# Kernel tuning notes

Measured on AMD Instinct MI355X. Metric: run time of the kernel, lower is better.

## Reference

```python
import jax, jax.numpy as jnp
import numpy as np

BN_EPS = 1e-5


def _guide_net(fullres, w1, b1, bn_gamma, bn_beta, bn_mean, bn_var, w2, b2):
    # two 1x1 convs == channel matmuls
    x = jnp.einsum('nchw,oc->nohw', fullres, w1[:, :, 0, 0]) + b1[None, :, None, None]
    inv = bn_gamma / jnp.sqrt(bn_var + BN_EPS)
    x = (x - bn_mean[None, :, None, None]) * inv[None, :, None, None] + bn_beta[None, :, None, None]
    x = jax.nn.relu(x)
    g = jnp.einsum('nchw,oc->nohw', x, w2[:, :, 0, 0]) + b2[None, :, None, None]
    return jax.nn.sigmoid(g)  # [N,1,H,W] in (0,1)


def _slice_one(grid_n, guide_n):
    # grid_n: [C,D,h,w]; guide_n: [H,W]; trilinear grid_sample, align_corners=True.
    C, D, h, w = grid_n.shape
    H, W = guide_n.shape
    # normalized coords in torch code map exactly to voxel coords [0, size-1]
    gz = guide_n * (D - 1)                      # per-pixel depth coord [H,W]
    z0f = jnp.floor(gz)
    tz = (gz - z0f)[None, :, :]                 # [1,H,W]
    z0 = jnp.clip(z0f, 0, D - 1).astype(jnp.int32)
    z1 = jnp.clip(z0f + 1, 0, D - 1).astype(jnp.int32)
    gy = jnp.linspace(0.0, h - 1.0, H)
    y0f = jnp.floor(gy)
    ty = (gy - y0f)[None, :, None]              # [1,H,1]
    y0 = jnp.clip(y0f, 0, h - 1).astype(jnp.int32)[:, None]
    y1 = jnp.clip(y0f + 1, 0, h - 1).astype(jnp.int32)[:, None]
    gx = jnp.linspace(0.0, w - 1.0, W)
    x0f = jnp.floor(gx)
    tx = (gx - x0f)[None, None, :]              # [1,1,W]
    x0 = jnp.clip(x0f, 0, w - 1).astype(jnp.int32)[None, :]
    x1 = jnp.clip(x0f + 1, 0, w - 1).astype(jnp.int32)[None, :]

    def g(z, y, x):
        # z:[H,W], y:[H,1], x:[1,W] -> broadcast gather -> [C,H,W]
        return grid_n[:, z, y, x]

    def lerp_xy(z):
        a = g(z, y0, x0) * (1 - tx) + g(z, y0, x1) * tx
        b = g(z, y1, x0) * (1 - tx) + g(z, y1, x1) * tx
        return a * (1 - ty) + b * ty

    return lerp_xy(z0) * (1 - tz) + lerp_xy(z1) * tz  # [C,H,W]


def _apply_coeffs(coeff, fullres):
    # coeff: [N,12,H,W]; rows (0:3,+3), (4:7,+7), (8:11,+11)
    N, _, H, W = coeff.shape
    A = coeff[:, jnp.array([0, 1, 2, 4, 5, 6, 8, 9, 10])].reshape(N, 3, 3, H, W)
    bias = coeff[:, jnp.array([3, 7, 11])]
    return jnp.einsum('nkchw,nchw->nkhw', A, fullres) + bias


def setup_inputs() -> dict:
    key = jax.random.key(0)
    ks = jax.random.split(key, 10)
    N, H, W = 2, 1080, 1920
    return {
        'fullres': jax.random.uniform(ks[0], (N, 3, H, W), jnp.float32),
        'bilateral_grid': jax.random.normal(ks[1], (N, 12, 8, 16, 16), jnp.float32),
        'w1': jax.random.normal(ks[2], (16, 3, 1, 1), jnp.float32) * 0.2,
        'b1': jax.random.normal(ks[3], (16,), jnp.float32) * 0.1,
        'bn_gamma': jax.random.uniform(ks[4], (16,), jnp.float32, 0.5, 1.5),
        'bn_beta': jax.random.normal(ks[5], (16,), jnp.float32) * 0.1,
        'bn_mean': jax.random.normal(ks[6], (16,), jnp.float32) * 0.1,
        'bn_var': jax.random.uniform(ks[7], (16,), jnp.float32, 0.5, 1.5),
        'w2': jax.random.normal(ks[8], (1, 16, 1, 1), jnp.float32) * 0.2,
        'b2': jax.random.normal(ks[9], (1,), jnp.float32) * 0.1,
    }


def reference(fullres, bilateral_grid, w1, b1, bn_gamma, bn_beta, bn_mean, bn_var, w2, b2):
    guide = _guide_net(fullres, w1, b1, bn_gamma, bn_beta, bn_mean, bn_var, w2, b2)  # [N,1,H,W]
    coeff = jax.vmap(_slice_one)(bilateral_grid, guide[:, 0])                         # [N,12,H,W]
    return _apply_coeffs(coeff, fullres)                                              # [N,3,H,W]
```

## Files before the change

### kernel.cpp

```cpp
#include <hip/hip_runtime.h>
#include <hip/hip_bf16.h>
#include <math.h>

#define HWV (1080 * 1920)

typedef _Float16 half2 __attribute__((ext_vector_type(2)));
typedef __fp16   pk2   __attribute__((ext_vector_type(2)));
union U32H2 { unsigned u; half2 h; pk2 p; };

__global__ void prep_w(const float* __restrict__ w1, const float* __restrict__ b1,
                       const float* __restrict__ gamma, const float* __restrict__ beta,
                       const float* __restrict__ mean, const float* __restrict__ var,
                       const float* __restrict__ w2, const float* __restrict__ b2,
                       float* __restrict__ wsw) {
    int i = threadIdx.x;
    if (i < 16) {
        float inv = gamma[i] / sqrtf(var[i] + 1e-5f);
        float wr = w1[i*3+0] * inv, wg = w1[i*3+1] * inv, wb = w1[i*3+2] * inv;
        float bs = (b1[i] - mean[i]) * inv + beta[i];
        wsw[64 + i] = w2[i];
        unsigned* wp = (unsigned*)(wsw + 84);
        U32H2 t;
        t.p = __builtin_amdgcn_cvt_pkrtz(wr, wr); wp[i*4+0] = t.u;
        t.p = __builtin_amdgcn_cvt_pkrtz(wg, wg); wp[i*4+1] = t.u;
        t.p = __builtin_amdgcn_cvt_pkrtz(wb, wb); wp[i*4+2] = t.u;
        t.p = __builtin_amdgcn_cvt_pkrtz(bs, bs); wp[i*4+3] = t.u;
    }
    if (i == 0) wsw[80] = b2[0];
}

__global__ __launch_bounds__(512, 8) void fused_kernel(
        const float* __restrict__ fullres,
        const float* __restrict__ grid,
        const float* __restrict__ wsw,
        float* __restrict__ out) {
    __shared__ unsigned slo[9][9][4];
    __shared__ unsigned shi[9][9][2];

    const int tid = threadIdx.x;
    const int n   = blockIdx.z;
    const int y   = blockIdx.y;
    const int xs  = blockIdx.x * 1024;
    const int x   = xs + 2 * tid;
    const bool act = (x < 1920);

    const int p = y * 1920 + min(x, 1918);
    const float* fr = fullres + n * 3 * HWV + p;
    float2 R = *(const float2*)(fr);
    float2 G = *(const float2*)(fr + HWV);
    float2 B = *(const float2*)(fr + 2 * HWV);

    const int a = (int)((float)xs * (15.0f / 1919.0f));
    {
        float gy = (float)y * (15.0f / 1079.0f);
        float y0f = floorf(gy);
        float ty = gy - y0f;
        int y0 = min((int)y0f, 15);
        int y1 = min(y0 + 1, 15);
        const int dy = (y1 - y0) * 16;
        const float* gb = grid + n * 24576 + y0 * 16;
        if (tid < 486) {
            int j   = tid / 81;
            int rem = tid - j * 81;
            int z   = rem / 9;
            int k   = rem - z * 9;
            int zz  = min(z, 7);
            int xc  = min(a + k, 15);
            const float* q0 = gb + (2 * j) * 2048 + zz * 256 + xc;
            const float* q1 = q0 + 2048;
            float v00 = q0[0], v01 = q0[dy];
            float v10 = q1[0], v11 = q1[dy];
            float e0 = fmaf(ty, v01 - v00, v00);
            float e1 = fmaf(ty, v11 - v10, v10);
            U32H2 t;
            t.p = __builtin_amdgcn_cvt_pkrtz(e0, e1);
            if (j < 4) slo[k][z][j] = t.u;
            else       shi[k][z][j - 4] = t.u;
        }
    }
    __syncthreads();

    if (!act) return;

    U32H2 rr, gg, bb;
    rr.p = __builtin_amdgcn_cvt_pkrtz(R.x, R.y);
    gg.p = __builtin_amdgcn_cvt_pkrtz(G.x, G.y);
    bb.p = __builtin_amdgcn_cvt_pkrtz(B.x, B.y);
    const unsigned* wp = (const unsigned*)(wsw + 84);
    const half2 zero = {(_Float16)0.0f, (_Float16)0.0f};
    float b2s = wsw[80];
    float acc0 = b2s, acc1 = b2s;
#pragma unroll
    for (int c = 0; c < 16; ++c) {
        U32H2 wr, wg, wb, bs;
        wr.u = wp[4*c+0]; wg.u = wp[4*c+1]; wb.u = wp[4*c+2]; bs.u = wp[4*c+3];
        half2 h = wr.h * rr.h + (wg.h * gg.h + (wb.h * bb.h + bs.h));
        h = __builtin_elementwise_max(h, zero);
        float w2c = wsw[64 + c];
        acc0 = fmaf((float)h.x, w2c, acc0);
        acc1 = fmaf((float)h.y, w2c, acc1);
    }

    float accv[2] = {acc0, acc1};
    float rv[2] = {R.x, R.y}, gv[2] = {G.x, G.y}, bv[2] = {B.x, B.y};
    float outr[2], outg[2], outb[2];

#pragma unroll
    for (int q = 0; q < 2; ++q) {
        float e = __expf(-accv[q]);
        float guide = __builtin_amdgcn_rcpf(1.0f + e);
        float gz = guide * 7.0f;
        float z0f = floorf(gz);
        float tz = gz - z0f;
        int z0 = min((int)z0f, 7);
        int z1 = z0 + 1;

        float gx = (float)(x + q) * (15.0f / 1919.0f);
        float x0f = floorf(gx);
        float tx = gx - x0f;
        int x0 = (int)x0f;
        int k0 = x0 - a;
        int k1 = min(x0 + 1, 15) - a;

        float wx0 = 1.0f - tx, wx1 = tx;
        float wz0 = 1.0f - tz, wz1 = tz;

        U32H2 w00h, w01h, w10h, w11h;
        w00h.p = __builtin_amdgcn_cvt_pkrtz(wx0 * wz0, wx0 * wz0);
        w01h.p = __builtin_amdgcn_cvt_pkrtz(wx0 * wz1, wx0 * wz1);
        w10h.p = __builtin_amdgcn_cvt_pkrtz(wx1 * wz0, wx1 * wz0);
        w11h.p = __builtin_amdgcn_cvt_pkrtz(wx1 * wz1, wx1 * wz1);

        const uint4 A0 = *(const uint4*)&slo[k0][z0][0];
        const uint4 A1 = *(const uint4*)&slo[k0][z1][0];
        const uint4 B0 = *(const uint4*)&slo[k1][z0][0];
        const uint4 B1 = *(const uint4*)&slo[k1][z1][0];
        const uint2 C0 = *(const uint2*)&shi[k0][z0][0];
        const uint2 C1 = *(const uint2*)&shi[k0][z1][0];
        const uint2 D0 = *(const uint2*)&shi[k1][z0][0];
        const uint2 D1 = *(const uint2*)&shi[k1][z1][0];

        unsigned a0j[6] = {A0.x, A0.y, A0.z, A0.w, C0.x, C0.y};
        unsigned a1j[6] = {A1.x, A1.y, A1.z, A1.w, C1.x, C1.y};
        unsigned b0j[6] = {B0.x, B0.y, B0.z, B0.w, D0.x, D0.y};
        unsigned b1j[6] = {B1.x, B1.y, B1.z, B1.w, D1.x, D1.y};

        half2 hc[6];
#pragma unroll
        for (int j = 0; j < 6; ++j) {
            U32H2 ua0, ua1, ub0, ub1;
            ua0.u = a0j[j]; ua1.u = a1j[j]; ub0.u = b0j[j]; ub1.u = b1j[j];
            half2 h = w00h.h * ua0.h + (w01h.h * ua1.h);
            h = w10h.h * ub0.h + h;
            h = w11h.h * ub1.h + h;
            hc[j] = h;
        }

        outr[q] = fmaf((float)hc[0].x, rv[q], fmaf((float)hc[0].y, gv[q],
                  fmaf((float)hc[1].x, bv[q], (float)hc[1].y)));
        outg[q] = fmaf((float)hc[2].x, rv[q], fmaf((float)hc[2].y, gv[q],
                  fmaf((float)hc[3].x, bv[q], (float)hc[3].y)));
        outb[q] = fmaf((float)hc[4].x, rv[q], fmaf((float)hc[4].y, gv[q],
                  fmaf((float)hc[5].x, bv[q], (float)hc[5].y)));
    }

    float* op = out + n * 3 * HWV + p;
    *(float2*)(op)           = make_float2(outr[0], outr[1]);
    *(float2*)(op + HWV)     = make_float2(outg[0], outg[1]);
    *(float2*)(op + 2 * HWV) = make_float2(outb[0], outb[1]);
}

extern "C" void kernel_launch(void* const* d_in, const int* in_sizes, int n_in,
                              void* d_out, int out_size, void* d_ws, size_t ws_size,
                              hipStream_t stream) {
    const float* fullres = (const float*)d_in[0];
    const float* grid    = (const float*)d_in[1];
    const float* w1      = (const float*)d_in[2];
    const float* b1      = (const float*)d_in[3];
    const float* gamma   = (const float*)d_in[4];
    const float* beta    = (const float*)d_in[5];
    const float* mean    = (const float*)d_in[6];
    const float* var     = (const float*)d_in[7];
    const float* w2      = (const float*)d_in[8];
    const float* b2      = (const float*)d_in[9];
    float* out = (float*)d_out;

    float* wsw = (float*)d_ws;

    prep_w<<<1, 64, 0, stream>>>(w1, b1, gamma, beta, mean, var, w2, b2, wsw);

    dim3 grid_dim(2, 1080, 2);
    fused_kernel<<<grid_dim, 512, 0, stream>>>(fullres, grid, wsw, out);
}
```

Baseline: 32.25 us.

## Process four rows per block with double-buffered grid slice and prefetch

Each block now handles four image rows instead of one. While computing the current row, it prefetches the next row's pixels and grid samples into a second shared-memory buffer. This amortizes block launch and setup, and hides global load latency behind compute. In exchange there are four times fewer blocks, an extra barrier per row, and more register pressure from the prefetched values.

```diff
diff --git a/kernel.cpp b/kernel.cpp
--- a/kernel.cpp
+++ b/kernel.cpp
@@ -3,6 +3,7 @@
 #include <math.h>
 
 #define HWV (1080 * 1920)
+#define NROWS 4
 
 typedef _Float16 half2 __attribute__((ext_vector_type(2)));
 typedef __fp16   pk2   __attribute__((ext_vector_type(2)));
@@ -34,140 +35,178 @@
         const float* __restrict__ grid,
         const float* __restrict__ wsw,
         float* __restrict__ out) {
-    __shared__ unsigned slo[9][9][4];
-    __shared__ unsigned shi[9][9][2];
+    __shared__ unsigned slo[2][9][9][4];
+    __shared__ unsigned shi[2][9][9][2];
 
     const int tid = threadIdx.x;
-    const int n   = blockIdx.z;
-    const int y   = blockIdx.y;
-    const int xs  = blockIdx.x * 1024;
+    const int seg = blockIdx.x;
+    const int n   = blockIdx.y;
+    const int yb  = blockIdx.z * NROWS;
+    const int xs  = seg * 1024;
     const int x   = xs + 2 * tid;
     const bool act = (x < 1920);
-
-    const int p = y * 1920 + min(x, 1918);
-    const float* fr = fullres + n * 3 * HWV + p;
-    float2 R = *(const float2*)(fr);
-    float2 G = *(const float2*)(fr + HWV);
-    float2 B = *(const float2*)(fr + 2 * HWV);
-
     const int a = (int)((float)xs * (15.0f / 1919.0f));
-    {
+    const int pcol = min(x, 1918);
+
+    const bool sact = (tid < 486);
+    int sj = 0, sz = 0, sk = 0;
+    const float* sq0 = grid;
+    if (sact) {
+        sj = tid / 81;
+        int rem = tid - sj * 81;
+        sz = rem / 9;
+        sk = rem - sz * 9;
+        int szz = min(sz, 7);
+        int sxc = min(a + sk, 15);
+        sq0 = grid + n * 24576 + (2 * sj) * 2048 + szz * 256 + sxc;
+    }
+
+    float sv0, sv1, sv2, sv3, sty;
+    auto stage_load = [&](int y) {
         float gy = (float)y * (15.0f / 1079.0f);
         float y0f = floorf(gy);
-        float ty = gy - y0f;
+        sty = gy - y0f;
         int y0 = min((int)y0f, 15);
         int y1 = min(y0 + 1, 15);
-        const int dy = (y1 - y0) * 16;
-        const float* gb = grid + n * 24576 + y0 * 16;
-        if (tid < 486) {
-            int j   = tid / 81;
-            int rem = tid - j * 81;
-            int z   = rem / 9;
-            int k   = rem - z * 9;
-            int zz  = min(z, 7);
-            int xc  = min(a + k, 15);
-            const float* q0 = gb + (2 * j) * 2048 + zz * 256 + xc;
-            const float* q1 = q0 + 2048;
-            float v00 = q0[0], v01 = q0[dy];
-            float v10 = q1[0], v11 = q1[dy];
-            float e0 = fmaf(ty, v01 - v00, v00);
-            float e1 = fmaf(ty, v11 - v10, v10);
+        if (sact) {
+            const float* q0 = sq0 + y0 * 16;
+            int dy = (y1 - y0) * 16;
+            sv0 = q0[0];    sv1 = q0[dy];
+            sv2 = q0[2048]; sv3 = q0[2048 + dy];
+        }
+    };
+    auto stage_write = [&](int buf) {
+        if (sact) {
+            float e0 = fmaf(sty, sv1 - sv0, sv0);
+            float e1 = fmaf(sty, sv3 - sv2, sv2);
             U32H2 t;
             t.p = __builtin_amdgcn_cvt_pkrtz(e0, e1);
-            if (j < 4) slo[k][z][j] = t.u;
-            else       shi[k][z][j - 4] = t.u;
-        }
-    }
-    __syncthreads();
-
-    if (!act) return;
-
-    U32H2 rr, gg, bb;
-    rr.p = __builtin_amdgcn_cvt_pkrtz(R.x, R.y);
-    gg.p = __builtin_amdgcn_cvt_pkrtz(G.x, G.y);
-    bb.p = __builtin_amdgcn_cvt_pkrtz(B.x, B.y);
+            if (sj < 4) slo[buf][sk][sz][sj] = t.u;
+            else        shi[buf][sk][sz][sj - 4] = t.u;
+        }
+    };
+    auto fr_load = [&](int y, float2& R, float2& G, float2& B) {
+        const float* fr = fullres + n * 3 * HWV + y * 1920 + pcol;
+        R = *(const float2*)(fr);
+        G = *(const float2*)(fr + HWV);
+        B = *(const float2*)(fr + 2 * HWV);
+    };
+
     const unsigned* wp = (const unsigned*)(wsw + 84);
     const half2 zero = {(_Float16)0.0f, (_Float16)0.0f};
-    float b2s = wsw[80];
-    float acc0 = b2s, acc1 = b2s;
-#pragma unroll
-    for (int c = 0; c < 16; ++c) {
-        U32H2 wr, wg, wb, bs;
-        wr.u = wp[4*c+0]; wg.u = wp[4*c+1]; wb.u = wp[4*c+2]; bs.u = wp[4*c+3];
-        half2 h = wr.h * rr.h + (wg.h * gg.h + (wb.h * bb.h + bs.h));
-        h = __builtin_elementwise_max(h, zero);
-        float w2c = wsw[64 + c];
-        acc0 = fmaf((float)h.x, w2c, acc0);
-        acc1 = fmaf((float)h.y, w2c, acc1);
+    const float b2s = wsw[80];
+
+    float2 R, G, B;
+    stage_load(yb);
+    fr_load(yb, R, G, B);
+    stage_write(0);
+    __syncthreads();
+
+    int cur = 0;
+#pragma unroll
+    for (int rrow = 0; rrow < NROWS; ++rrow) {
+        const int y = yb + rrow;
+        const int p = y * 1920 + pcol;
+
+        float2 Rn, Gn, Bn;
+        if (rrow + 1 < NROWS) {
+            stage_load(y + 1);
+            fr_load(y + 1, Rn, Gn, Bn);
+        }
+
+        if (act) {
+            U32H2 rr, gg, bb;
+            rr.p = __builtin_amdgcn_cvt_pkrtz(R.x, R.y);
+            gg.p = __builtin_amdgcn_cvt_pkrtz(G.x, G.y);
+            bb.p = __builtin_amdgcn_cvt_pkrtz(B.x, B.y);
+            float acc0 = b2s, acc1 = b2s;
+#pragma unroll
+            for (int c = 0; c < 16; ++c) {
+                U32H2 wr, wg, wb, bs;
+                wr.u = wp[4*c+0]; wg.u = wp[4*c+1]; wb.u = wp[4*c+2]; bs.u = wp[4*c+3];
+                half2 h = wr.h * rr.h + (wg.h * gg.h + (wb.h * bb.h + bs.h));
+                h = __builtin_elementwise_max(h, zero);
+                float w2c = wsw[64 + c];
+                acc0 = fmaf((float)h.x, w2c, acc0);
+                acc1 = fmaf((float)h.y, w2c, acc1);
+            }
+
+            float accv[2] = {acc0, acc1};
+            float rv[2] = {R.x, R.y}, gv[2] = {G.x, G.y}, bv[2] = {B.x, B.y};
+            float outr[2], outg[2], outb[2];
+
+#pragma unroll
+            for (int q = 0; q < 2; ++q) {
+                float e = __expf(-accv[q]);
+                float guide = __builtin_amdgcn_rcpf(1.0f + e);
+                float gz = guide * 7.0f;
+                float z0f = floorf(gz);
+                float tz = gz - z0f;
+                int z0 = min((int)z0f, 7);
+                int z1 = z0 + 1;
+
+                float gx = (float)(x + q) * (15.0f / 1919.0f);
+                float x0f = floorf(gx);
+                float tx = gx - x0f;
+                int x0 = (int)x0f;
+                int k0 = x0 - a;
+                int k1 = min(x0 + 1, 15) - a;
+
+                float wx0 = 1.0f - tx, wx1 = tx;
+                float wz0 = 1.0f - tz, wz1 = tz;
+
+                U32H2 w00h, w01h, w10h, w11h;
+                w00h.p = __builtin_amdgcn_cvt_pkrtz(wx0 * wz0, wx0 * wz0);
+                w01h.p = __builtin_amdgcn_cvt_pkrtz(wx0 * wz1, wx0 * wz1);
+                w10h.p = __builtin_amdgcn_cvt_pkrtz(wx1 * wz0, wx1 * wz0);
+                w11h.p = __builtin_amdgcn_cvt_pkrtz(wx1 * wz1, wx1 * wz1);
+
+                const uint4 A0 = *(const uint4*)&slo[cur][k0][z0][0];
+                const uint4 A1 = *(const uint4*)&slo[cur][k0][z1][0];
+                const uint4 B0 = *(const uint4*)&slo[cur][k1][z0][0];
+                const uint4 B1 = *(const uint4*)&slo[cur][k1][z1][0];
+                const uint2 C0 = *(const uint2*)&shi[cur][k0][z0][0];
+                const uint2 C1 = *(const uint2*)&shi[cur][k0][z1][0];
+                const uint2 D0 = *(const uint2*)&shi[cur][k1][z0][0];
+                const uint2 D1 = *(const uint2*)&shi[cur][k1][z1][0];
+
+                unsigned a0j[6] = {A0.x, A0.y, A0.z, A0.w, C0.x, C0.y};
+                unsigned a1j[6] = {A1.x, A1.y, A1.z, A1.w, C1.x, C1.y};
+                unsigned b0j[6] = {B0.x, B0.y, B0.z, B0.w, D0.x, D0.y};
+                unsigned b1j[6] = {B1.x, B1.y, B1.z, B1.w, D1.x, D1.y};
+
+                half2 hc[6];
+#pragma unroll
+                for (int j = 0; j < 6; ++j) {
+                    U32H2 ua0, ua1, ub0, ub1;
+                    ua0.u = a0j[j]; ua1.u = a1j[j]; ub0.u = b0j[j]; ub1.u = b1j[j];
+                    half2 h = w00h.h * ua0.h + (w01h.h * ua1.h);
+                    h = w10h.h * ub0.h + h;
+                    h = w11h.h * ub1.h + h;
+                    hc[j] = h;
+                }
+
+                outr[q] = fmaf((float)hc[0].x, rv[q], fmaf((float)hc[0].y, gv[q],
+                          fmaf((float)hc[1].x, bv[q], (float)hc[1].y)));
+                outg[q] = fmaf((float)hc[2].x, rv[q], fmaf((float)hc[2].y, gv[q],
+                          fmaf((float)hc[3].x, bv[q], (float)hc[3].y)));
+                outb[q] = fmaf((float)hc[4].x, rv[q], fmaf((float)hc[4].y, gv[q],
+                          fmaf((float)hc[5].x, bv[q], (float)hc[5].y)));
+            }
+
+            float* op = out + n * 3 * HWV + p;
+            *(float2*)(op)           = make_float2(outr[0], outr[1]);
+            *(float2*)(op + HWV)     = make_float2(outg[0], outg[1]);
+            *(float2*)(op + 2 * HWV) = make_float2(outb[0], outb[1]);
+        }
+
+        if (rrow + 1 < NROWS) {
+            stage_write(cur ^ 1);
+        }
+        __syncthreads();
+        cur ^= 1;
+        R = Rn; G = Gn; B = Bn;
     }
-
-    float accv[2] = {acc0, acc1};
-    float rv[2] = {R.x, R.y}, gv[2] = {G.x, G.y}, bv[2] = {B.x, B.y};
-    float outr[2], outg[2], outb[2];
-
-#pragma unroll
-    for (int q = 0; q < 2; ++q) {
-        float e = __expf(-accv[q]);
-        float guide = __builtin_amdgcn_rcpf(1.0f + e);
-        float gz = guide * 7.0f;
-        float z0f = floorf(gz);
-        float tz = gz - z0f;
-        int z0 = min((int)z0f, 7);
-        int z1 = z0 + 1;
-
-        float gx = (float)(x + q) * (15.0f / 1919.0f);
-        float x0f = floorf(gx);
-        float tx = gx - x0f;
-        int x0 = (int)x0f;
-        int k0 = x0 - a;
-        int k1 = min(x0 + 1, 15) - a;
-
-        float wx0 = 1.0f - tx, wx1 = tx;
-        float wz0 = 1.0f - tz, wz1 = tz;
-
-        U32H2 w00h, w01h, w10h, w11h;
-        w00h.p = __builtin_amdgcn_cvt_pkrtz(wx0 * wz0, wx0 * wz0);
-        w01h.p = __builtin_amdgcn_cvt_pkrtz(wx0 * wz1, wx0 * wz1);
-        w10h.p = __builtin_amdgcn_cvt_pkrtz(wx1 * wz0, wx1 * wz0);
-        w11h.p = __builtin_amdgcn_cvt_pkrtz(wx1 * wz1, wx1 * wz1);
-
-        const uint4 A0 = *(const uint4*)&slo[k0][z0][0];
-        const uint4 A1 = *(const uint4*)&slo[k0][z1][0];
-        const uint4 B0 = *(const uint4*)&slo[k1][z0][0];
-        const uint4 B1 = *(const uint4*)&slo[k1][z1][0];
-        const uint2 C0 = *(const uint2*)&shi[k0][z0][0];
-        const uint2 C1 = *(const uint2*)&shi[k0][z1][0];
-        const uint2 D0 = *(const uint2*)&shi[k1][z0][0];
-        const uint2 D1 = *(const uint2*)&shi[k1][z1][0];
-
-        unsigned a0j[6] = {A0.x, A0.y, A0.z, A0.w, C0.x, C0.y};
-        unsigned a1j[6] = {A1.x, A1.y, A1.z, A1.w, C1.x, C1.y};
-        unsigned b0j[6] = {B0.x, B0.y, B0.z, B0.w, D0.x, D0.y};
-        unsigned b1j[6] = {B1.x, B1.y, B1.z, B1.w, D1.x, D1.y};
-
-        half2 hc[6];
-#pragma unroll
-        for (int j = 0; j < 6; ++j) {
-            U32H2 ua0, ua1, ub0, ub1;
-            ua0.u = a0j[j]; ua1.u = a1j[j]; ub0.u = b0j[j]; ub1.u = b1j[j];
-            half2 h = w00h.h * ua0.h + (w01h.h * ua1.h);
-            h = w10h.h * ub0.h + h;
-            h = w11h.h * ub1.h + h;
-            hc[j] = h;
-        }
-
-        outr[q] = fmaf((float)hc[0].x, rv[q], fmaf((float)hc[0].y, gv[q],
-                  fmaf((float)hc[1].x, bv[q], (float)hc[1].y)));
-        outg[q] = fmaf((float)hc[2].x, rv[q], fmaf((float)hc[2].y, gv[q],
-                  fmaf((float)hc[3].x, bv[q], (float)hc[3].y)));
-        outb[q] = fmaf((float)hc[4].x, rv[q], fmaf((float)hc[4].y, gv[q],
-                  fmaf((float)hc[5].x, bv[q], (float)hc[5].y)));
-    }
-
-    float* op = out + n * 3 * HWV + p;
-    *(float2*)(op)           = make_float2(outr[0], outr[1]);
-    *(float2*)(op + HWV)     = make_float2(outg[0], outg[1]);
-    *(float2*)(op + 2 * HWV) = make_float2(outb[0], outb[1]);
 }
 
 extern "C" void kernel_launch(void* const* d_in, const int* in_sizes, int n_in,
@@ -189,6 +228,6 @@
 
     prep_w<<<1, 64, 0, stream>>>(w1, b1, gamma, beta, mean, var, w2, b2, wsw);
 
-    dim3 grid_dim(2, 1080, 2);
+    dim3 grid_dim(2, 2, 1080 / NROWS);
     fused_kernel<<<grid_dim, 512, 0, stream>>>(fullres, grid, wsw, out);
 }
```

Result: slower. 35.86 us (+11.2%).

## Process one full image row per 960-thread block instead of two half-row blocks

Applied to the files above, without the earlier changes.

Each block now covers a whole 1920-pixel row with 960 threads, so the grid goes from 2x1080x2 blocks of 512 threads to 1080x2 blocks. The shared y-interpolated grid slice grows to all 16 x columns, filled by 864 threads, and the per-block x offset and the inactive-thread early exit are removed. This halves the per-block grid staging and removes the wasted threads in the second half-row block. In exchange, blocks are larger, the occupancy hint is dropped, and each block does more staging work before its barrier.

```diff
diff --git a/kernel.cpp b/kernel.cpp
--- a/kernel.cpp
+++ b/kernel.cpp
@@ -29,28 +29,25 @@
     if (i == 0) wsw[80] = b2[0];
 }
 
-__global__ __launch_bounds__(512, 8) void fused_kernel(
+__global__ __launch_bounds__(960) void fused_kernel(
         const float* __restrict__ fullres,
         const float* __restrict__ grid,
         const float* __restrict__ wsw,
         float* __restrict__ out) {
-    __shared__ unsigned slo[9][9][4];
-    __shared__ unsigned shi[9][9][2];
+    __shared__ unsigned slo[16][9][4];
+    __shared__ unsigned shi[16][9][2];
 
     const int tid = threadIdx.x;
-    const int n   = blockIdx.z;
-    const int y   = blockIdx.y;
-    const int xs  = blockIdx.x * 1024;
-    const int x   = xs + 2 * tid;
-    const bool act = (x < 1920);
+    const int y   = blockIdx.x;
+    const int n   = blockIdx.y;
+    const int x   = 2 * tid;
+    const int p   = y * 1920 + x;
 
-    const int p = y * 1920 + min(x, 1918);
     const float* fr = fullres + n * 3 * HWV + p;
     float2 R = *(const float2*)(fr);
     float2 G = *(const float2*)(fr + HWV);
     float2 B = *(const float2*)(fr + 2 * HWV);
 
-    const int a = (int)((float)xs * (15.0f / 1919.0f));
     {
         float gy = (float)y * (15.0f / 1079.0f);
         float y0f = floorf(gy);
@@ -59,14 +56,13 @@
         int y1 = min(y0 + 1, 15);
         const int dy = (y1 - y0) * 16;
         const float* gb = grid + n * 24576 + y0 * 16;
-        if (tid < 486) {
-            int j   = tid / 81;
-            int rem = tid - j * 81;
-            int z   = rem / 9;
-            int k   = rem - z * 9;
+        if (tid < 864) {
+            int k   = tid / 54;
+            int rem = tid - k * 54;
+            int z   = rem / 6;
+            int j   = rem - z * 6;
             int zz  = min(z, 7);
-            int xc  = min(a + k, 15);
-            const float* q0 = gb + (2 * j) * 2048 + zz * 256 + xc;
+            const float* q0 = gb + (2 * j) * 2048 + zz * 256 + k;
             const float* q1 = q0 + 2048;
             float v00 = q0[0], v01 = q0[dy];
             float v10 = q1[0], v11 = q1[dy];
@@ -80,15 +76,13 @@
     }
     __syncthreads();
 
-    if (!act) return;
-
     U32H2 rr, gg, bb;
     rr.p = __builtin_amdgcn_cvt_pkrtz(R.x, R.y);
     gg.p = __builtin_amdgcn_cvt_pkrtz(G.x, G.y);
     bb.p = __builtin_amdgcn_cvt_pkrtz(B.x, B.y);
     const unsigned* wp = (const unsigned*)(wsw + 84);
     const half2 zero = {(_Float16)0.0f, (_Float16)0.0f};
-    float b2s = wsw[80];
+    const float b2s = wsw[80];
     float acc0 = b2s, acc1 = b2s;
 #pragma unroll
     for (int c = 0; c < 16; ++c) {
@@ -118,9 +112,8 @@
         float gx = (float)(x + q) * (15.0f / 1919.0f);
         float x0f = floorf(gx);
         float tx = gx - x0f;
-        int x0 = (int)x0f;
-        int k0 = x0 - a;
-        int k1 = min(x0 + 1, 15) - a;
+        int k0 = (int)x0f;
+        int k1 = min(k0 + 1, 15);
 
         float wx0 = 1.0f - tx, wx1 = tx;
         float wz0 = 1.0f - tz, wz1 = tz;
@@ -189,6 +182,6 @@
 
     prep_w<<<1, 64, 0, stream>>>(w1, b1, gamma, beta, mean, var, w2, b2, wsw);
 
-    dim3 grid_dim(2, 1080, 2);
-    fused_kernel<<<grid_dim, 512, 0, stream>>>(fullres, grid, wsw, out);
+    dim3 grid_dim(1080, 2);
+    fused_kernel<<<grid_dim, 960, 0, stream>>>(fullres, grid, wsw, out);
 }
```

New measurement: 40.44 us. 1.25x slower.

## Fold weight prep into fused kernel and broadcast weights via LDS and readlane

Applied to the files above, without the earlier changes.

Removes the separate prep_w launch: each block's spare threads compute the folded BN/conv1 weights into shared memory alongside the grid slice staging. Weights are then loaded once per lane from LDS and broadcast with readlane instead of scalar global loads. The grid dimension order is also permuted so the batch index is adjacent to the x-segment. It saves one kernel launch and the dependency between launches, at the cost of redundant per-block weight computation and extra readlane instructions.

```diff
diff --git a/kernel.cpp b/kernel.cpp
--- a/kernel.cpp
+++ b/kernel.cpp
@@ -7,98 +7,108 @@
 typedef _Float16 half2 __attribute__((ext_vector_type(2)));
 typedef __fp16   pk2   __attribute__((ext_vector_type(2)));
 union U32H2 { unsigned u; half2 h; pk2 p; };
-
-__global__ void prep_w(const float* __restrict__ w1, const float* __restrict__ b1,
-                       const float* __restrict__ gamma, const float* __restrict__ beta,
-                       const float* __restrict__ mean, const float* __restrict__ var,
-                       const float* __restrict__ w2, const float* __restrict__ b2,
-                       float* __restrict__ wsw) {
-    int i = threadIdx.x;
-    if (i < 16) {
-        float inv = gamma[i] / sqrtf(var[i] + 1e-5f);
-        float wr = w1[i*3+0] * inv, wg = w1[i*3+1] * inv, wb = w1[i*3+2] * inv;
-        float bs = (b1[i] - mean[i]) * inv + beta[i];
-        wsw[64 + i] = w2[i];
-        unsigned* wp = (unsigned*)(wsw + 84);
-        U32H2 t;
-        t.p = __builtin_amdgcn_cvt_pkrtz(wr, wr); wp[i*4+0] = t.u;
-        t.p = __builtin_amdgcn_cvt_pkrtz(wg, wg); wp[i*4+1] = t.u;
-        t.p = __builtin_amdgcn_cvt_pkrtz(wb, wb); wp[i*4+2] = t.u;
-        t.p = __builtin_amdgcn_cvt_pkrtz(bs, bs); wp[i*4+3] = t.u;
-    }
-    if (i == 0) wsw[80] = b2[0];
-}
+union U32F  { unsigned u; float f; };
 
 __global__ __launch_bounds__(512, 8) void fused_kernel(
         const float* __restrict__ fullres,
         const float* __restrict__ grid,
-        const float* __restrict__ wsw,
+        const float* __restrict__ w1,
+        const float* __restrict__ b1,
+        const float* __restrict__ bn_gamma,
+        const float* __restrict__ bn_beta,
+        const float* __restrict__ bn_mean,
+        const float* __restrict__ bn_var,
+        const float* __restrict__ w2,
+        const float* __restrict__ b2,
         float* __restrict__ out) {
     __shared__ unsigned slo[9][9][4];
     __shared__ unsigned shi[9][9][2];
+    __shared__ unsigned wlds[81];
 
     const int tid = threadIdx.x;
-    const int n   = blockIdx.z;
-    const int y   = blockIdx.y;
-    const int xs  = blockIdx.x * 1024;
+    const int seg = blockIdx.x;
+    const int n   = blockIdx.y;
+    const int y   = blockIdx.z;
+    const int xs  = seg * 1024;
     const int x   = xs + 2 * tid;
     const bool act = (x < 1920);
-
-    const int p = y * 1920 + min(x, 1918);
+    const int a = (int)((float)xs * (15.0f / 1919.0f));
+    const int pcol = min(x, 1918);
+    const int p = y * 1920 + pcol;
+
     const float* fr = fullres + n * 3 * HWV + p;
     float2 R = *(const float2*)(fr);
     float2 G = *(const float2*)(fr + HWV);
     float2 B = *(const float2*)(fr + 2 * HWV);
 
-    const int a = (int)((float)xs * (15.0f / 1919.0f));
-    {
+    if (tid < 486) {
         float gy = (float)y * (15.0f / 1079.0f);
         float y0f = floorf(gy);
         float ty = gy - y0f;
         int y0 = min((int)y0f, 15);
         int y1 = min(y0 + 1, 15);
         const int dy = (y1 - y0) * 16;
-        const float* gb = grid + n * 24576 + y0 * 16;
-        if (tid < 486) {
-            int j   = tid / 81;
-            int rem = tid - j * 81;
-            int z   = rem / 9;
-            int k   = rem - z * 9;
-            int zz  = min(z, 7);
-            int xc  = min(a + k, 15);
-            const float* q0 = gb + (2 * j) * 2048 + zz * 256 + xc;
-            const float* q1 = q0 + 2048;
-            float v00 = q0[0], v01 = q0[dy];
-            float v10 = q1[0], v11 = q1[dy];
-            float e0 = fmaf(ty, v01 - v00, v00);
-            float e1 = fmaf(ty, v11 - v10, v10);
-            U32H2 t;
-            t.p = __builtin_amdgcn_cvt_pkrtz(e0, e1);
-            if (j < 4) slo[k][z][j] = t.u;
-            else       shi[k][z][j - 4] = t.u;
-        }
+        int j   = tid / 81;
+        int rem = tid - j * 81;
+        int z   = rem / 9;
+        int k   = rem - z * 9;
+        int zz  = min(z, 7);
+        int xc  = min(a + k, 15);
+        const float* q0 = grid + n * 24576 + (2 * j) * 2048 + zz * 256 + y0 * 16 + xc;
+        const float* q1 = q0 + 2048;
+        float v00 = q0[0], v01 = q0[dy];
+        float v10 = q1[0], v11 = q1[dy];
+        float e0 = fmaf(ty, v01 - v00, v00);
+        float e1 = fmaf(ty, v11 - v10, v10);
+        U32H2 t;
+        t.p = __builtin_amdgcn_cvt_pkrtz(e0, e1);
+        if (j < 4) slo[k][z][j] = t.u;
+        else       shi[k][z][j - 4] = t.u;
+    } else if (tid < 502) {
+        int c = tid - 486;
+        float inv = bn_gamma[c] * __builtin_amdgcn_rcpf(sqrtf(bn_var[c] + 1e-5f));
+        float wrf = w1[c*3+0] * inv;
+        float wgf = w1[c*3+1] * inv;
+        float wbf = w1[c*3+2] * inv;
+        float bsf = fmaf(b1[c] - bn_mean[c], inv, bn_beta[c]);
+        U32H2 t;
+        t.p = __builtin_amdgcn_cvt_pkrtz(wrf, wrf); wlds[4*c+0] = t.u;
+        t.p = __builtin_amdgcn_cvt_pkrtz(wgf, wgf); wlds[4*c+1] = t.u;
+        t.p = __builtin_amdgcn_cvt_pkrtz(wbf, wbf); wlds[4*c+2] = t.u;
+        t.p = __builtin_amdgcn_cvt_pkrtz(bsf, bsf); wlds[4*c+3] = t.u;
+        U32F u; u.f = w2[c];
+        wlds[64 + c] = u.u;
+    } else if (tid == 502) {
+        U32F u; u.f = b2[0];
+        wlds[80] = u.u;
     }
     __syncthreads();
 
     if (!act) return;
+
+    const int l = tid & 63;
+    unsigned v0 = wlds[l];
+    unsigned v1 = wlds[64 + min(l, 16)];
 
     U32H2 rr, gg, bb;
     rr.p = __builtin_amdgcn_cvt_pkrtz(R.x, R.y);
     gg.p = __builtin_amdgcn_cvt_pkrtz(G.x, G.y);
     bb.p = __builtin_amdgcn_cvt_pkrtz(B.x, B.y);
-    const unsigned* wp = (const unsigned*)(wsw + 84);
     const half2 zero = {(_Float16)0.0f, (_Float16)0.0f};
-    float b2s = wsw[80];
-    float acc0 = b2s, acc1 = b2s;
+    U32F b2u; b2u.u = (unsigned)__builtin_amdgcn_readlane((int)v1, 16);
+    float acc0 = b2u.f, acc1 = b2u.f;
 #pragma unroll
     for (int c = 0; c < 16; ++c) {
         U32H2 wr, wg, wb, bs;
-        wr.u = wp[4*c+0]; wg.u = wp[4*c+1]; wb.u = wp[4*c+2]; bs.u = wp[4*c+3];
+        wr.u = (unsigned)__builtin_amdgcn_readlane((int)v0, 4*c+0);
+        wg.u = (unsigned)__builtin_amdgcn_readlane((int)v0, 4*c+1);
+        wb.u = (unsigned)__builtin_amdgcn_readlane((int)v0, 4*c+2);
+        bs.u = (unsigned)__builtin_amdgcn_readlane((int)v0, 4*c+3);
         half2 h = wr.h * rr.h + (wg.h * gg.h + (wb.h * bb.h + bs.h));
         h = __builtin_elementwise_max(h, zero);
-        float w2c = wsw[64 + c];
-        acc0 = fmaf((float)h.x, w2c, acc0);
-        acc1 = fmaf((float)h.y, w2c, acc1);
+        U32F w2u; w2u.u = (unsigned)__builtin_amdgcn_readlane((int)v1, c);
+        acc0 = fmaf((float)h.x, w2u.f, acc0);
+        acc1 = fmaf((float)h.y, w2u.f, acc1);
     }
 
     float accv[2] = {acc0, acc1};
@@ -185,10 +195,7 @@
     const float* b2      = (const float*)d_in[9];
     float* out = (float*)d_out;
 
-    float* wsw = (float*)d_ws;
-
-    prep_w<<<1, 64, 0, stream>>>(w1, b1, gamma, beta, mean, var, w2, b2, wsw);
-
-    dim3 grid_dim(2, 1080, 2);
-    fused_kernel<<<grid_dim, 512, 0, stream>>>(fullres, grid, wsw, out);
+    dim3 grid_dim(2, 2, 1080);
+    fused_kernel<<<grid_dim, 512, 0, stream>>>(fullres, grid, w1, b1, gamma,
+                                               beta, mean, var, w2, b2, out);
 }
```

Result: slower. 33.67 us (+4.4%).
